# Optimization experiments

Hardware: AMD Instinct MI355X
Metric: run time of the kernel (lower is better)

Reference implementation:

```python
import jax, jax.numpy as jnp
import numpy as np

# Model config (matches init_kwargs)
D_MODEL = 512
D_STATE = 64
D_CONV = 4
EXPAND = 2
NHEADS = 16
HEADDIM = 64
D_INNER = EXPAND * D_MODEL          # 1024 == NHEADS * HEADDIM
D_IN_PROJ = 2 * D_INNER + 2 * D_STATE + NHEADS  # 2192
BATCH = 2
SEQLEN = 2048


def setup_inputs() -> dict:
    key = jax.random.key(0)
    ks = jax.random.split(key, 5)
    s = 0.02  # weight scale so activations stay well-conditioned
    return {
        "x": jax.random.normal(ks[0], (BATCH, SEQLEN, D_MODEL), jnp.float32),
        "W_in": jax.random.normal(ks[1], (D_IN_PROJ, D_MODEL), jnp.float32) * s,
        "conv_w": jax.random.normal(ks[2], (D_INNER, 1, D_CONV), jnp.float32) * 0.3,
        "conv_b": jnp.zeros((D_INNER,), jnp.float32),
        "A_log": jnp.zeros((NHEADS,), jnp.float32),       # torch init: log(ones)=0
        "dt_bias": jnp.ones((NHEADS,), jnp.float32),
        "W_out": jax.random.normal(ks[3], (D_MODEL, D_INNER), jnp.float32) * s,
    }


def reference(x, W_in, conv_w, conv_b, A_log, dt_bias, W_out):
    b, l, _ = x.shape
    # in_proj (no bias)
    proj = jnp.einsum('bld,ed->ble', x, W_in)  # [b, l, D_IN_PROJ]
    z, xs, B, C, dt = jnp.split(
        proj, [D_INNER, 2 * D_INNER, 2 * D_INNER + D_STATE, 2 * D_INNER + 2 * D_STATE], axis=-1)

    # depthwise causal conv1d: torch pads (d_conv-1) on both sides then truncates
    # right to seqlen, equivalent to left-padding by d_conv-1.
    xc = jax.lax.conv_general_dilated(
        xs.transpose(0, 2, 1), conv_w,
        window_strides=(1,), padding=[(D_CONV - 1, 0)],
        dimension_numbers=('NCH', 'OIH', 'NCH'),
        feature_group_count=D_INNER)
    xc = xc + conv_b[None, :, None]
    x_ssm = jax.nn.silu(xc).transpose(0, 2, 1)           # [b, l, D_INNER]
    xh = x_ssm.reshape(b, l, NHEADS, HEADDIM)            # [b, l, h, p]

    dt = jax.nn.softplus(dt + dt_bias)                   # [b, l, h]
    A = -jnp.exp(A_log)                                  # [h]
    dA = jnp.exp(dt * A)                                 # [b, l, h], in (0,1)

    # sequential selective scan over time (lax.scan), state h: [b, h, n, p]
    def step(h, inp):
        dAt, Bt, Ct, xt = inp                            # [b,h],[b,n],[b,n],[b,h,p]
        h = dAt[:, :, None, None] * h + jnp.einsum('bn,bhp->bhnp', Bt, xt)
        y = jnp.einsum('bn,bhnp->bhp', Ct, h)
        return h, y

    h0 = jnp.zeros((b, NHEADS, D_STATE, HEADDIM), x.dtype)
    _, ys = jax.lax.scan(step, h0, (dA.transpose(1, 0, 2),
                                    B.transpose(1, 0, 2),
                                    C.transpose(1, 0, 2),
                                    xh.transpose(1, 0, 2, 3)))
    y = ys.transpose(1, 0, 2, 3).reshape(b, l, D_INNER)  # [b, l, d_inner]

    y = y * jax.nn.silu(z)                               # gated output
    return jnp.einsum('ble,de->bld', y, W_out)           # out_proj (no bias)
```

## Files before the change

kernel.cpp:

```cpp
#include <hip/hip_runtime.h>
#include <cstdint>
#include <cstddef>

#define B_N     2
#define L_N     2048
#define DMODEL  512
#define DINNER  1024
#define DSTATE  64
#define NHEADS  16
#define EPROJ   2192
#define PB      2176
#define OFF_Z   0
#define OFF_XP  1024
#define OFF_B   2048
#define OFF_C   2112
#define LC      64
#define NC      32

typedef unsigned short u16;
typedef unsigned int   u32;
typedef __attribute__((ext_vector_type(8))) short short8;
typedef __attribute__((ext_vector_type(4))) float floatx4;

__device__ __forceinline__ float silu_f(float v) { return v / (1.f + __expf(-v)); }

__device__ __forceinline__ u16 f2bf(float f) {
    union { float f; uint32_t u; } v; v.f = f;
    uint32_t r = (v.u + 0x7FFFu + ((v.u >> 16) & 1u)) >> 16;
    return (u16)r;
}

__device__ __forceinline__ float bf2f(u16 b) {
    union { u32 u; float f; } v; v.u = (u32)b << 16; return v.f;
}

__device__ __forceinline__ u32 pack2(float lo, float hi) {
    return (u32)f2bf(lo) | ((u32)f2bf(hi) << 16);
}

__device__ __forceinline__ float lane_bcast(float v, int n) {
    union { float f; uint32_t u; } a, b;
    a.f = v;
    b.u = __builtin_amdgcn_readlane(a.u, n);
    return b.f;
}

__device__ __forceinline__ short8 frag_ld(const u32* s, int row, int k0) {
    const u32* q = s + row * 33 + (k0 >> 1);
    union { u32 u[4]; short8 v; } r;
    r.u[0] = q[0]; r.u[1] = q[1]; r.u[2] = q[2]; r.u[3] = q[3];
    return r.v;
}

__device__ __forceinline__ void gload_lds16(const u16* g, u16* s) {
    __builtin_amdgcn_global_load_lds(
        (const __attribute__((address_space(1))) void*)g,
        (__attribute__((address_space(3))) void*)s,
        16, 0, 0);
}

__global__ __launch_bounds__(256) void cast3_kern(
    const float* __restrict__ s0, u16* __restrict__ d0, int n0,
    const float* __restrict__ s1, u16* __restrict__ d1, int n1,
    const float* __restrict__ s2, u16* __restrict__ d2, int n2)
{
    int i = blockIdx.x * 256 + threadIdx.x;
    const float* s; u16* d;
    if (i < n0)           { s = s0; d = d0; }
    else if (i < n0 + n1) { i -= n0; s = s1; d = d1; }
    else                  { i -= n0 + n1; if (i >= n2) return; s = s2; d = d2; }
    float4 v = ((const float4*)s)[i];
    ushort4 o;
    o.x = f2bf(v.x); o.y = f2bf(v.y); o.z = f2bf(v.z); o.w = f2bf(v.w);
    ((ushort4*)d)[i] = o;
}

template<int BM, int BN, bool GUARD, bool PSPLIT>
__global__ __launch_bounds__(256, 2) void gemm_mfma_bt(
    const u16* __restrict__ A, const u16* __restrict__ Bt,
    float* __restrict__ Cf, u16* __restrict__ Cb, float* __restrict__ Dt,
    int M, int N, int K)
{
    constexpr int MI = BM / 32;
    constexpr int NI = BN / 32;
    __shared__ u16 As[2][BM * 32];
    __shared__ u16 Bs[2][BN * 32];

    const int tid = threadIdx.x;
    const int w   = tid >> 6;
    const int ln  = tid & 63;
    const int wm  = w >> 1, wn = w & 1;
    const int bm  = blockIdx.y * BM;
    const int bn  = blockIdx.x * BN;

    const int srow = ln >> 2;
    const int skq  = (ln & 3) * 8;
    const int fr = ln & 15;
    const int fq = (ln >> 4) * 8;

    floatx4 acc[MI][NI];
    const floatx4 fzero = {0.f, 0.f, 0.f, 0.f};
    #pragma unroll
    for (int mi = 0; mi < MI; ++mi)
        #pragma unroll
        for (int ni = 0; ni < NI; ++ni) acc[mi][ni] = fzero;

    for (int k0 = 0; k0 < K; k0 += 64) {
        #pragma unroll
        for (int p = 0; p < 2; ++p) {
            const int kp = k0 + p * 32;
            #pragma unroll
            for (int g = 0; g < BM / 16; ++g) {
                if ((g & 3) != w) continue;
                gload_lds16(A + (size_t)(bm + g * 16 + srow) * K + kp + skq,
                            &As[p][g * 16 * 32]);
            }
            #pragma unroll
            for (int g = 0; g < BN / 16; ++g) {
                if ((g & 3) != w) continue;
                int rn = bn + g * 16 + srow;
                if (GUARD) rn = (rn < N) ? rn : (N - 1);
                gload_lds16(Bt + (size_t)rn * K + kp + skq,
                            &Bs[p][g * 16 * 32]);
            }
        }
        __syncthreads();

        #pragma unroll
        for (int p = 0; p < 2; ++p) {
            short8 af[MI], bf[NI];
            #pragma unroll
            for (int mi = 0; mi < MI; ++mi)
                af[mi] = *(const short8*)&As[p][(wm * (BM / 2) + mi * 16 + fr) * 32 + fq];
            #pragma unroll
            for (int ni = 0; ni < NI; ++ni)
                bf[ni] = *(const short8*)&Bs[p][(wn * (BN / 2) + ni * 16 + fr) * 32 + fq];
            #pragma unroll
            for (int mi = 0; mi < MI; ++mi)
                #pragma unroll
                for (int ni = 0; ni < NI; ++ni)
                    acc[mi][ni] = __builtin_amdgcn_mfma_f32_16x16x32_bf16(
                        af[mi], bf[ni], acc[mi][ni], 0, 0, 0);
        }
        __syncthreads();
    }

    const int cr = (ln >> 4) * 4;
    const int cc = ln & 15;
    #pragma unroll
    for (int mi = 0; mi < MI; ++mi) {
        const int row0 = bm + wm * (BM / 2) + mi * 16 + cr;
        #pragma unroll
        for (int ni = 0; ni < NI; ++ni) {
            const int col = bn + wn * (BN / 2) + ni * 16 + cc;
            #pragma unroll
            for (int r = 0; r < 4; ++r) {
                const int row = row0 + r;
                const float v = acc[mi][ni][r];
                if (PSPLIT) {
                    if (col < PB)
                        Cb[(size_t)row * PB + col] = f2bf(v);
                    else if (col < EPROJ)
                        Dt[(size_t)row * 16 + (col - PB)] = v;
                } else {
                    Cf[(size_t)row * N + col] = v;
                }
            }
        }
    }
}

__global__ __launch_bounds__(256) void ssd_phase1(
    const u16* __restrict__ projb, const float* __restrict__ dtf,
    const float* __restrict__ cw, const float* __restrict__ cb,
    const float* __restrict__ A_log, const float* __restrict__ dt_bias,
    float* __restrict__ hl, float* __restrict__ Pc, float* __restrict__ LaBuf,
    u32* __restrict__ xT)
{
    __shared__ u32 sBD[64 * 33];
    __shared__ u32 sXt[64 * 33];

    const int bid = blockIdx.x;
    const int c = bid & (NC - 1);
    const int h = (bid >> 5) & (NHEADS - 1);
    const int b = bid >> 9;
    const int tid = threadIdx.x;
    const int w = tid >> 6, ln = tid & 63;
    const int a = ln & 15, q = ln >> 4;
    const size_t r0 = (size_t)b * L_N + c * LC;

    float dt = dtf[(r0 + ln) * 16 + h] + dt_bias[h];
    float sp = (dt > 15.f) ? dt : log1pf(__expf(dt));
    float La = sp * (-__expf(A_log[h]));
    #pragma unroll
    for (int d = 1; d < 64; d <<= 1) {
        float up = __shfl_up(La, d, 64);
        if (ln >= d) La += up;
    }
    if (w == 0) LaBuf[(size_t)bid * 64 + ln] = La;
    const float La63 = lane_bcast(La, 63);

    const int ch = h * 64 + ln;
    const float4 w4 = *(const float4*)(cw + ch * 4);
    const float bias = cb[ch];
    const u16* xcol = projb + OFF_XP + ch;
    const size_t bbase = (size_t)b * L_N;

    float xr[3];
    #pragma unroll
    for (int i = 0; i < 3; ++i) {
        const int tl = c * LC + 16 * w - 3 + i;
        xr[i] = (tl >= 0) ? bf2f(xcol[(bbase + tl) * PB]) : 0.f;
    }

    #pragma unroll
    for (int j = 0; j < 8; ++j) {
        const int sp_ = w * 8 + j, s = sp_ * 2;
        const float xa = bf2f(xcol[(r0 + s) * PB]);
        const float xb = bf2f(xcol[(r0 + s + 1) * PB]);
        float a0 = bias, a1 = bias;
        a0 += xr[0] * w4.x; a0 += xr[1] * w4.y; a0 += xr[2] * w4.z; a0 += xa * w4.w;
        a1 += xr[1] * w4.x; a1 += xr[2] * w4.y; a1 += xa * w4.z;   a1 += xb * w4.w;
        xr[0] = xr[2]; xr[1] = xa; xr[2] = xb;
        const float x0 = silu_f(a0), x1 = silu_f(a1);
        const u32 xp = pack2(x0, x1);
        sXt[ln * 33 + sp_] = xp;
        xT[(size_t)bid * 2048 + sp_ * 64 + ln] = xp;
        const float w0 = __expf(La63 - lane_bcast(La, s));
        const float w1 = __expf(La63 - lane_bcast(La, s + 1));
        const float b0 = bf2f(projb[(r0 + s) * PB + OFF_B + ln]) * w0;
        const float b1 = bf2f(projb[(r0 + s + 1) * PB + OFF_B + ln]) * w1;
        sBD[ln * 33 + sp_] = pack2(b0, b1);
    }
    __syncthreads();

    short8 af[2], bf[4][2];
    #pragma unroll
    for (int ks = 0; ks < 2; ++ks)
        af[ks] = frag_ld(sBD, w * 16 + a, ks * 32 + q * 8);
    #pragma unroll
    for (int tn = 0; tn < 4; ++tn)
        #pragma unroll
        for (int ks = 0; ks < 2; ++ks)
            bf[tn][ks] = frag_ld(sXt, tn * 16 + a, ks * 32 + q * 8);

    const floatx4 fzero = {0.f, 0.f, 0.f, 0.f};
    floatx4 acc[4];
    #pragma unroll
    for (int tn = 0; tn < 4; ++tn) {
        acc[tn] = fzero;
        #pragma unroll
        for (int ks = 0; ks < 2; ++ks)
            acc[tn] = __builtin_amdgcn_mfma_f32_16x16x32_bf16(
                af[ks], bf[tn][ks], acc[tn], 0, 0, 0);
    }

    float* hp = hl + (size_t)bid * (DSTATE * 64);
    #pragma unroll
    for (int tn = 0; tn < 4; ++tn)
        #pragma unroll
        for (int r = 0; r < 4; ++r)
            hp[(w * 16 + q * 4 + r) * 64 + tn * 16 + a] = acc[tn][r];
    if (tid == 0) Pc[bid] = __expf(La63);
}

__global__ __launch_bounds__(256) void ssd_phase2(
    float* __restrict__ hl, const float* __restrict__ Pc)
{
    const int bid = blockIdx.x;
    const int bh = bid >> 4;
    const int e = (bid & 15) * 256 + threadIdx.x;
    const size_t base = (size_t)(bh * NC) * 4096 + e;

    float v[NC];
    #pragma unroll
    for (int c = 0; c < NC; ++c)
        v[c] = hl[base + (size_t)c * 4096];

    float carry = 0.f;
    #pragma unroll
    for (int c = 0; c < NC; ++c) {
        const float cur = v[c];
        v[c] = carry;
        carry = fmaf(Pc[bh * NC + c], carry, cur);
    }

    #pragma unroll
    for (int c = 0; c < NC; ++c)
        hl[base + (size_t)c * 4096] = v[c];
}

__global__ __launch_bounds__(256) void ssd_phase3(
    const u16* __restrict__ projb, const u32* __restrict__ xT,
    const float* __restrict__ hl, const float* __restrict__ LaBuf,
    u16* __restrict__ yz)
{
    __shared__ char lds[34048];
    u32* sBW   = (u32*)lds;
    u32* sC    = (u32*)(lds + 8448);
    u32* sXt   = (u32*)(lds + 16896);
    u32* sH    = (u32*)(lds + 25344);
    float* sLaF = (float*)(lds + 33792);
    float* sY  = (float*)(lds + 8448);

    const int bid = blockIdx.x;
    const int c = bid & (NC - 1);
    const int h = (bid >> 5) & (NHEADS - 1);
    const int b = bid >> 9;
    const int tid = threadIdx.x;
    const int w = tid >> 6, ln = tid & 63;
    const int a = ln & 15, q = ln >> 4;
    const int hw = ln >> 5, k32 = ln & 31;
    const size_t r0 = (size_t)b * L_N + c * LC;

    if (tid < 64) sLaF[tid] = LaBuf[(size_t)bid * 64 + tid];

    const float* hs = hl + (size_t)bid * 4096;
    #pragma unroll
    for (int j = 0; j < 8; ++j) {
        const int rp = w * 8 + j;
        const int row = rp * 2 + hw;
        sBW[row * 33 + k32] = *(const u32*)(projb + (r0 + row) * PB + OFF_B + 2 * k32);
        sC [row * 33 + k32] = *(const u32*)(projb + (r0 + row) * PB + OFF_C + 2 * k32);
        sXt[ln * 33 + rp] = xT[(size_t)bid * 2048 + rp * 64 + ln];
        sH [ln * 33 + rp] = pack2(hs[(2 * rp) * 64 + ln], hs[(2 * rp + 1) * 64 + ln]);
    }
    __syncthreads();

    const floatx4 fzero = {0.f, 0.f, 0.f, 0.f};

    short8 cfr[2], bfr[4][2];
    #pragma unroll
    for (int ks = 0; ks < 2; ++ks)
        cfr[ks] = frag_ld(sC, w * 16 + a, ks * 32 + q * 8);
    #pragma unroll
    for (int tm = 0; tm < 4; ++tm)
        if (tm <= w)
            #pragma unroll
            for (int ks = 0; ks < 2; ++ks)
                bfr[tm][ks] = frag_ld(sBW, tm * 16 + a, ks * 32 + q * 8);
    floatx4 accS[4];
    #pragma unroll
    for (int tm = 0; tm < 4; ++tm) {
        if (tm > w) continue;
        accS[tm] = fzero;
        #pragma unroll
        for (int ks = 0; ks < 2; ++ks)
            accS[tm] = __builtin_amdgcn_mfma_f32_16x16x32_bf16(
                bfr[tm][ks], cfr[ks], accS[tm], 0, 0, 0);
    }
    __syncthreads();

    {
        const int i = w * 16 + a;
        const float Li = sLaF[i];
        #pragma unroll
        for (int tm = 0; tm < 4; ++tm) {
            const int d0 = i * 33 + tm * 8 + q * 2;
            if (tm > w) {
                sBW[d0] = 0; sBW[d0 + 1] = 0;
            } else {
                const float4 Ls = *(const float4*)(sLaF + tm * 16 + q * 4);
                float v[4];
                #pragma unroll
                for (int r = 0; r < 4; ++r) {
                    const int s = tm * 16 + q * 4 + r;
                    const float ww = (s <= i) ? __expf(Li - ((const float*)&Ls)[r]) : 0.f;
                    v[r] = accS[tm][r] * ww;
                }
                sBW[d0]     = pack2(v[0], v[1]);
                sBW[d0 + 1] = pack2(v[2], v[3]);
            }
        }
    }

    short8 hfr[4][2];
    #pragma unroll
    for (int tp = 0; tp < 4; ++tp)
        #pragma unroll
        for (int ks = 0; ks < 2; ++ks)
            hfr[tp][ks] = frag_ld(sH, tp * 16 + a, ks * 32 + q * 8);
    floatx4 accY[4];
    #pragma unroll
    for (int tp = 0; tp < 4; ++tp) {
        accY[tp] = fzero;
        #pragma unroll
        for (int ks = 0; ks < 2; ++ks)
            accY[tp] = __builtin_amdgcn_mfma_f32_16x16x32_bf16(
                cfr[ks], hfr[tp][ks], accY[tp], 0, 0, 0);
    }
    {
        const float4 Ls = *(const float4*)(sLaF + w * 16 + q * 4);
        float e4[4];
        #pragma unroll
        for (int r = 0; r < 4; ++r) e4[r] = __expf(((const float*)&Ls)[r]);
        #pragma unroll
        for (int tp = 0; tp < 4; ++tp)
            #pragma unroll
            for (int r = 0; r < 4; ++r) accY[tp][r] *= e4[r];
    }

    short8 wfr[2], xfr[4][2];
    #pragma unroll
    for (int ks = 0; ks < 2; ++ks)
        wfr[ks] = frag_ld(sBW, w * 16 + a, ks * 32 + q * 8);
    #pragma unroll
    for (int tp = 0; tp < 4; ++tp)
        #pragma unroll
        for (int ks = 0; ks < 2; ++ks)
            xfr[tp][ks] = frag_ld(sXt, tp * 16 + a, ks * 32 + q * 8);
    #pragma unroll
    for (int tp = 0; tp < 4; ++tp)
        #pragma unroll
        for (int ks = 0; ks < 2; ++ks)
            accY[tp] = __builtin_amdgcn_mfma_f32_16x16x32_bf16(
                wfr[ks], xfr[tp][ks], accY[tp], 0, 0, 0);
    __syncthreads();

    #pragma unroll
    for (int tp = 0; tp < 4; ++tp)
        #pragma unroll
        for (int r = 0; r < 4; ++r)
            sY[(w * 16 + q * 4 + r) * 66 + tp * 16 + a] = accY[tp][r];
    #pragma unroll
    for (int ii = 0; ii < 16; ++ii) {
        const int i = w * 16 + ii;
        const float y = sY[i * 66 + ln];
        const float z = bf2f(projb[(r0 + i) * PB + OFF_Z + h * 64 + ln]);
        yz[(r0 + i) * DINNER + h * 64 + ln] = f2bf(y * silu_f(z));
    }
}

extern "C" void kernel_launch(void* const* d_in, const int* in_sizes, int n_in,
                              void* d_out, int out_size, void* d_ws, size_t ws_size,
                              hipStream_t stream)
{
    const float* x       = (const float*)d_in[0];
    const float* W_in    = (const float*)d_in[1];
    const float* conv_w  = (const float*)d_in[2];
    const float* conv_b  = (const float*)d_in[3];
    const float* A_log   = (const float*)d_in[4];
    const float* dt_bias = (const float*)d_in[5];
    const float* W_out   = (const float*)d_in[6];
    float* out = (float*)d_out;

    u16*   projb = (u16*)d_ws;
    float* dtf   = (float*)(projb + (size_t)4096 * PB);
    float* hl    = dtf + (size_t)4096 * 16;
    float* Pc    = hl + (size_t)1024 * 4096;
    float* LaBuf = Pc + 1024;
    u16*   xbf   = (u16*)(LaBuf + 1024 * 64);
    u16*   wibf  = xbf + (size_t)4096 * DMODEL;
    u16*   wobf  = wibf + (size_t)EPROJ * DMODEL;
    u16*   yzbf  = wobf + (size_t)DMODEL * DINNER;
    u32*   xT    = (u32*)(yzbf + (size_t)4096 * DINNER);

    const int M = B_N * L_N;
    const int n0 = M * DMODEL / 4, n1 = EPROJ * DMODEL / 4, n2 = DMODEL * DINNER / 4;

    cast3_kern<<<(n0 + n1 + n2 + 255) / 256, 256, 0, stream>>>(
        x, xbf, n0, W_in, wibf, n1, W_out, wobf, n2);

    gemm_mfma_bt<128, 160, true, true><<<dim3(14, M / 128), 256, 0, stream>>>(
        xbf, wibf, nullptr, projb, dtf, M, EPROJ, DMODEL);

    ssd_phase1<<<B_N * NHEADS * NC, 256, 0, stream>>>(
        projb, dtf, conv_w, conv_b, A_log, dt_bias, hl, Pc, LaBuf, xT);
    ssd_phase2<<<B_N * NHEADS * 16, 256, 0, stream>>>(hl, Pc);
    ssd_phase3<<<B_N * NHEADS * NC, 256, 0, stream>>>(
        projb, xT, hl, LaBuf, yzbf);

    gemm_mfma_bt<64, 64, false, false><<<dim3(DMODEL / 64, M / 64), 256, 0, stream>>>(
        yzbf, wobf, out, nullptr, nullptr, M, DMODEL, DINNER);
}
```

Baseline: 143.6 us.

## Store chunk states in bf16 and deepen GEMM K-staging to four panels

The per-chunk SSM states handed between phase1, phase2 and phase3 are now stored as bf16 instead of fp32. This halves the global traffic of the state buffer, and phase2 processes packed pairs with half as many blocks. Separately, the GEMM kernel gains a template parameter for the number of 32-wide K panels staged per sync, raised from 2 to 4 for both projections, which cuts barrier count but doubles LDS use and may reduce occupancy. The bf16 state storage adds rounding error to the inter-chunk carry.

```diff
diff --git a/kernel.cpp b/kernel.cpp
--- a/kernel.cpp
+++ b/kernel.cpp
@@ -75,7 +75,7 @@
     ((ushort4*)d)[i] = o;
 }
 
-template<int BM, int BN, bool GUARD, bool PSPLIT>
+template<int BM, int BN, int NP, bool GUARD, bool PSPLIT>
 __global__ __launch_bounds__(256, 2) void gemm_mfma_bt(
     const u16* __restrict__ A, const u16* __restrict__ Bt,
     float* __restrict__ Cf, u16* __restrict__ Cb, float* __restrict__ Dt,
@@ -83,8 +83,8 @@
 {
     constexpr int MI = BM / 32;
     constexpr int NI = BN / 32;
-    __shared__ u16 As[2][BM * 32];
-    __shared__ u16 Bs[2][BN * 32];
+    __shared__ u16 As[NP][BM * 32];
+    __shared__ u16 Bs[NP][BN * 32];
 
     const int tid = threadIdx.x;
     const int w   = tid >> 6;
@@ -105,9 +105,9 @@
         #pragma unroll
         for (int ni = 0; ni < NI; ++ni) acc[mi][ni] = fzero;
 
-    for (int k0 = 0; k0 < K; k0 += 64) {
-        #pragma unroll
-        for (int p = 0; p < 2; ++p) {
+    for (int k0 = 0; k0 < K; k0 += 32 * NP) {
+        #pragma unroll
+        for (int p = 0; p < NP; ++p) {
             const int kp = k0 + p * 32;
             #pragma unroll
             for (int g = 0; g < BM / 16; ++g) {
@@ -127,7 +127,7 @@
         __syncthreads();
 
         #pragma unroll
-        for (int p = 0; p < 2; ++p) {
+        for (int p = 0; p < NP; ++p) {
             short8 af[MI], bf[NI];
             #pragma unroll
             for (int mi = 0; mi < MI; ++mi)
@@ -174,7 +174,7 @@
     const u16* __restrict__ projb, const float* __restrict__ dtf,
     const float* __restrict__ cw, const float* __restrict__ cb,
     const float* __restrict__ A_log, const float* __restrict__ dt_bias,
-    float* __restrict__ hl, float* __restrict__ Pc, float* __restrict__ LaBuf,
+    u16* __restrict__ hb, float* __restrict__ Pc, float* __restrict__ LaBuf,
     u32* __restrict__ xT)
 {
     __shared__ u32 sBD[64 * 33];
@@ -255,44 +255,47 @@
                 af[ks], bf[tn][ks], acc[tn], 0, 0, 0);
     }
 
-    float* hp = hl + (size_t)bid * (DSTATE * 64);
+    u16* hp = hb + (size_t)bid * 4096;
     #pragma unroll
     for (int tn = 0; tn < 4; ++tn)
         #pragma unroll
         for (int r = 0; r < 4; ++r)
-            hp[(w * 16 + q * 4 + r) * 64 + tn * 16 + a] = acc[tn][r];
+            hp[(w * 16 + q * 4 + r) * 64 + tn * 16 + a] = f2bf(acc[tn][r]);
     if (tid == 0) Pc[bid] = __expf(La63);
 }
 
 __global__ __launch_bounds__(256) void ssd_phase2(
-    float* __restrict__ hl, const float* __restrict__ Pc)
+    u32* __restrict__ hb32, const float* __restrict__ Pc)
 {
     const int bid = blockIdx.x;
-    const int bh = bid >> 4;
-    const int e = (bid & 15) * 256 + threadIdx.x;
-    const size_t base = (size_t)(bh * NC) * 4096 + e;
-
-    float v[NC];
+    const int bh = bid >> 3;
+    const int e = (bid & 7) * 256 + threadIdx.x;
+    const size_t base = (size_t)(bh * NC) * 2048 + e;
+
+    u32 v[NC];
     #pragma unroll
     for (int c = 0; c < NC; ++c)
-        v[c] = hl[base + (size_t)c * 4096];
-
-    float carry = 0.f;
+        v[c] = hb32[base + (size_t)c * 2048];
+
+    float c0 = 0.f, c1 = 0.f;
     #pragma unroll
     for (int c = 0; c < NC; ++c) {
-        const float cur = v[c];
-        v[c] = carry;
-        carry = fmaf(Pc[bh * NC + c], carry, cur);
+        const u32 cur = v[c];
+        const float lo = bf2f((u16)cur), hi = bf2f((u16)(cur >> 16));
+        v[c] = pack2(c0, c1);
+        const float Pv = Pc[bh * NC + c];
+        c0 = fmaf(Pv, c0, lo);
+        c1 = fmaf(Pv, c1, hi);
     }
 
     #pragma unroll
     for (int c = 0; c < NC; ++c)
-        hl[base + (size_t)c * 4096] = v[c];
+        hb32[base + (size_t)c * 2048] = v[c];
 }
 
 __global__ __launch_bounds__(256) void ssd_phase3(
     const u16* __restrict__ projb, const u32* __restrict__ xT,
-    const float* __restrict__ hl, const float* __restrict__ LaBuf,
+    const u16* __restrict__ hb, const float* __restrict__ LaBuf,
     u16* __restrict__ yz)
 {
     __shared__ char lds[34048];
@@ -315,7 +318,7 @@
 
     if (tid < 64) sLaF[tid] = LaBuf[(size_t)bid * 64 + tid];
 
-    const float* hs = hl + (size_t)bid * 4096;
+    const u16* hs = hb + (size_t)bid * 4096;
     #pragma unroll
     for (int j = 0; j < 8; ++j) {
         const int rp = w * 8 + j;
@@ -323,7 +326,8 @@
         sBW[row * 33 + k32] = *(const u32*)(projb + (r0 + row) * PB + OFF_B + 2 * k32);
         sC [row * 33 + k32] = *(const u32*)(projb + (r0 + row) * PB + OFF_C + 2 * k32);
         sXt[ln * 33 + rp] = xT[(size_t)bid * 2048 + rp * 64 + ln];
-        sH [ln * 33 + rp] = pack2(hs[(2 * rp) * 64 + ln], hs[(2 * rp + 1) * 64 + ln]);
+        sH [ln * 33 + rp] = (u32)hs[(2 * rp) * 64 + ln]
+                          | ((u32)hs[(2 * rp + 1) * 64 + ln] << 16);
     }
     __syncthreads();
 
@@ -446,8 +450,8 @@
 
     u16*   projb = (u16*)d_ws;
     float* dtf   = (float*)(projb + (size_t)4096 * PB);
-    float* hl    = dtf + (size_t)4096 * 16;
-    float* Pc    = hl + (size_t)1024 * 4096;
+    u16*   hb    = (u16*)(dtf + (size_t)4096 * 16);
+    float* Pc    = (float*)(hb + (size_t)1024 * 4096);
     float* LaBuf = Pc + 1024;
     u16*   xbf   = (u16*)(LaBuf + 1024 * 64);
     u16*   wibf  = xbf + (size_t)4096 * DMODEL;
@@ -461,15 +465,15 @@
     cast3_kern<<<(n0 + n1 + n2 + 255) / 256, 256, 0, stream>>>(
         x, xbf, n0, W_in, wibf, n1, W_out, wobf, n2);
 
-    gemm_mfma_bt<128, 160, true, true><<<dim3(14, M / 128), 256, 0, stream>>>(
+    gemm_mfma_bt<128, 160, 4, true, true><<<dim3(14, M / 128), 256, 0, stream>>>(
         xbf, wibf, nullptr, projb, dtf, M, EPROJ, DMODEL);
 
     ssd_phase1<<<B_N * NHEADS * NC, 256, 0, stream>>>(
-        projb, dtf, conv_w, conv_b, A_log, dt_bias, hl, Pc, LaBuf, xT);
-    ssd_phase2<<<B_N * NHEADS * 16, 256, 0, stream>>>(hl, Pc);
+        projb, dtf, conv_w, conv_b, A_log, dt_bias, hb, Pc, LaBuf, xT);
+    ssd_phase2<<<B_N * NHEADS * 8, 256, 0, stream>>>((u32*)hb, Pc);
     ssd_phase3<<<B_N * NHEADS * NC, 256, 0, stream>>>(
-        projb, xT, hl, LaBuf, yzbf);
-
-    gemm_mfma_bt<64, 64, false, false><<<dim3(DMODEL / 64, M / 64), 256, 0, stream>>>(
+        projb, xT, hb, LaBuf, yzbf);
+
+    gemm_mfma_bt<64, 64, 4, false, false><<<dim3(DMODEL / 64, M / 64), 256, 0, stream>>>(
         yzbf, wobf, out, nullptr, nullptr, M, DMODEL, DINNER);
 }
```

Result: faster. 137.0 us (-4.6%).
